# Kernel tuning notes

Measured on AMD Instinct MI355X. Metric: run time of the kernel, lower is better.

## Reference

```python
import jax, jax.numpy as jnp
import numpy as np

B, S, D, H = 2, 4096, 1024, 16
DK = D // H


def setup_inputs() -> dict:
    key = jax.random.key(0)
    ks = jax.random.split(key, 8)
    q = jax.random.normal(ks[0], (B, S, D), dtype=jnp.float32)
    k = jax.random.normal(ks[1], (B, S, D), dtype=jnp.float32)
    v = jax.random.normal(ks[2], (B, S, D), dtype=jnp.float32)
    mask = jax.random.randint(ks[3], (1, 1, S, S), 0, 2, dtype=jnp.int32)
    # torch.nn.Linear weights, y = x @ W.T ; Kaiming-uniform-ish init scale
    lim = 1.0 / np.sqrt(D)
    Wq = jax.random.uniform(ks[4], (D, D), jnp.float32, -lim, lim)
    Wk = jax.random.uniform(ks[5], (D, D), jnp.float32, -lim, lim)
    Wv = jax.random.uniform(ks[6], (D, D), jnp.float32, -lim, lim)
    Wo = jax.random.uniform(ks[7], (D, D), jnp.float32, -lim, lim)
    return {"q": q, "k": k, "v": v, "mask": mask,
            "Wq": Wq, "Wk": Wk, "Wv": Wv, "Wo": Wo}


def reference(q, k, v, mask, Wq, Wk, Wv, Wo):
    # Linear projections (torch Linear: x @ W.T), split into heads [B,H,S,DK]
    def heads(x, W):
        return (x @ W.T).reshape(B, S, H, DK).transpose(0, 2, 1, 3)

    Q, K, V = heads(q, Wq), heads(k, Wk), heads(v, Wv)
    scale = 1.0 / jnp.sqrt(jnp.asarray(DK, dtype=Q.dtype))
    # [B,H,S,S] score matrix (original materializes it fully)
    scores = jnp.einsum("bhqd,bhkd->bhqk", Q, K) * scale
    # NOTE: original calls masked_fill without assignment -> mask is a no-op.
    # Dropout: eval-mode identity (original also references missing self.dropout).
    attn = jax.nn.softmax(scores, axis=-1)
    out = jnp.einsum("bhqk,bhkd->bhqd", attn, V)  # [B,H,S,DK]
    out = out.transpose(0, 2, 1, 3).reshape(B, S, D)
    return out @ Wo.T
```

## Files before the change

### kernel.cpp

```cpp
#include <hip/hip_runtime.h>
#include <cstdint>
#include <cstddef>

using u16 = unsigned short;
using u32 = unsigned int;

typedef _Float16 f16x8 __attribute__((ext_vector_type(8)));
typedef float    f32x4 __attribute__((ext_vector_type(4)));
typedef float    f32x16 __attribute__((ext_vector_type(16)));

#define MFMA16(a,b,c) __builtin_amdgcn_mfma_f32_16x16x32_f16((a),(b),(c),0,0,0)
#define MFMA32(a,b,c) __builtin_amdgcn_mfma_f32_32x32x16_f16((a),(b),(c),0,0,0)

__device__ __forceinline__ u16 f2h(float f) {
  return __builtin_bit_cast(u16, (_Float16)f);
}
__device__ __forceinline__ u32 pkrtz(float a, float b) {
  return __builtin_bit_cast(u32, __builtin_amdgcn_cvt_pkrtz(a, b));
}
__device__ __forceinline__ void plswap(u32 &a, u32 &b) {
  asm volatile("v_permlane32_swap_b32 %0, %1" : "+v"(a), "+v"(b));
}
__device__ __forceinline__ void async16(const void* g, void* lds) {
  __builtin_amdgcn_global_load_lds((const __attribute__((address_space(1))) void*)g,
                                   (__attribute__((address_space(3))) void*)lds,
                                   16, 0, 0);
}
#if __has_builtin(__builtin_amdgcn_exp2f)
__device__ __forceinline__ float exp2_hw(float x) { return __builtin_amdgcn_exp2f(x); }
#else
__device__ __forceinline__ float exp2_hw(float x) {
  float r; asm("v_exp_f32 %0, %1" : "=v"(r) : "v"(x)); return r;
}
#endif

__global__ __launch_bounds__(256) void cvt_f32_f16(const float* __restrict__ in,
                                                   u16* __restrict__ out, int n4,
                                                   float scale) {
  int i = blockIdx.x * 256 + threadIdx.x;
  const int stride = gridDim.x * 256;
  for (; i < n4; i += stride) {
    const float4 f = reinterpret_cast<const float4*>(in)[i];
    ushort4 o;
    o.x = f2h(f.x * scale); o.y = f2h(f.y * scale);
    o.z = f2h(f.z * scale); o.w = f2h(f.w * scale);
    reinterpret_cast<ushort4*>(out)[i] = o;
  }
}

template <int OF32>
__global__ __launch_bounds__(256) void gemm_bt(const u16* __restrict__ A,
                                               const u16* __restrict__ Bw,
                                               float* __restrict__ Cf,
                                               u16* __restrict__ Ch,
                                               int M, int N, int K) {
  __shared__ __align__(16) u16 Asm[128 * 64];
  __shared__ __align__(16) u16 Bsm[128 * 64];
  const int tid = threadIdx.x;
  const int w = tid >> 6, l = tid & 63;
  const int wr = w >> 1, wc = w & 1;
  const int m0 = blockIdx.y * 128, n0 = blockIdx.x * 128;
  const int lr = l >> 3, lc = l & 7, csrc = lc ^ lr;
  const int laneq = l & 15, laneg = l >> 4;
  f32x4 acc[4][4] = {};
  for (int k0 = 0; k0 < K; k0 += 64) {
    __syncthreads();
#pragma unroll
    for (int c = 0; c < 4; ++c) {
      const int row = c * 32 + w * 8 + lr;
      async16(A + (size_t)(m0 + row) * K + k0 + csrc * 8, &Asm[c * 2048 + w * 512]);
      async16(Bw + (size_t)(n0 + row) * K + k0 + csrc * 8, &Bsm[c * 2048 + w * 512]);
    }
    __syncthreads();
#pragma unroll
    for (int ks = 0; ks < 2; ++ks) {
      f16x8 af[4], bfr[4];
#pragma unroll
      for (int mi = 0; mi < 4; ++mi) {
        const int row = wr * 64 + mi * 16 + laneq;
        const int ch = (ks * 4 + laneg) ^ (row & 7);
        af[mi] = *(const f16x8*)&Asm[row * 64 + ch * 8];
      }
#pragma unroll
      for (int ni = 0; ni < 4; ++ni) {
        const int row = wc * 64 + ni * 16 + laneq;
        const int ch = (ks * 4 + laneg) ^ (row & 7);
        bfr[ni] = *(const f16x8*)&Bsm[row * 64 + ch * 8];
      }
#pragma unroll
      for (int mi = 0; mi < 4; ++mi)
#pragma unroll
        for (int ni = 0; ni < 4; ++ni)
          acc[mi][ni] = MFMA16(af[mi], bfr[ni], acc[mi][ni]);
    }
  }
#pragma unroll
  for (int mi = 0; mi < 4; ++mi)
#pragma unroll
    for (int r = 0; r < 4; ++r) {
      const int gm = m0 + wr * 64 + mi * 16 + laneg * 4 + r;
#pragma unroll
      for (int ni = 0; ni < 4; ++ni) {
        const int gn = n0 + wc * 64 + ni * 16 + laneq;
        if constexpr (OF32) Cf[(size_t)gm * N + gn] = acc[mi][ni][r];
        else                Ch[(size_t)gm * N + gn] = f2h(acc[mi][ni][r]);
      }
    }
}

__global__ __launch_bounds__(256) void transpose_v(const u16* __restrict__ Vp,
                                                   u16* __restrict__ VT) {
  __shared__ u16 t[64 * 66];
  const int tid = threadIdx.x;
  const int s0 = blockIdx.x * 64, bh = blockIdx.y;
  const int b = bh >> 4, h = bh & 15;
  const int r = tid >> 2;
  const u16* src = Vp + (size_t)(b * 4096 + s0 + r) * 1024 + h * 64;
#pragma unroll
  for (int i = 0; i < 2; ++i) {
    const int c = (tid & 3) + i * 4;
    union { uint4 u; u32 ww[4]; } vv;
    vv.u = *(const uint4*)(src + c * 8);
#pragma unroll
    for (int j = 0; j < 4; ++j)
      *(u32*)&t[r * 66 + c * 8 + j * 2] = vv.ww[j];
  }
  __syncthreads();
  const int dk = tid >> 2;
  u16* dst = VT + ((size_t)bh * 64 + dk) * 4096 + s0;
#pragma unroll
  for (int i = 0; i < 2; ++i) {
    const int sc = (tid & 3) + i * 4;
    union { uint4 u; u16 s[8]; } o;
#pragma unroll
    for (int j = 0; j < 8; ++j) o.s[j] = t[(sc * 8 + j) * 66 + dk];
    *(uint4*)(dst + sc * 8) = o.u;
  }
}

__global__ __launch_bounds__(256, 4) void attn_fwd(const u16* __restrict__ Qp,
                                                   const u16* __restrict__ Kp,
                                                   const u16* __restrict__ VT,
                                                   u16* __restrict__ AO) {
  union SM {
    struct { u16 K[2][64 * 64]; u16 V[2][64 * 64]; } st;
    u16 osm[4][32 * 72];
  };
  __shared__ __align__(16) SM sm;
  const int tid = threadIdx.x, w = tid >> 6, l = tid & 63;
  const int l31 = l & 31, hi = l >> 5, l7 = l & 7, lr = l >> 3;
  const int bid = blockIdx.x;
  const int slot = bid >> 3;
  const int bh = (bid & 7) * 4 + (slot >> 5), qx = slot & 31;
  const int b = bh >> 4, h = bh & 15;
  const int q0 = qx * 128;
  const size_t hb = (size_t)b * 4096 * 1024 + (size_t)h * 64;
  const u16* Kh = Kp + hb;
  const u16* Vh = VT + (size_t)bh * 64 * 4096;
  const int csrc = l7 ^ lr;

  f16x8 qf[4];
  {
    const u16* qp = Qp + hb + (size_t)(q0 + w * 32 + l31) * 1024 + hi * 8;
#pragma unroll
    for (int kk = 0; kk < 4; ++kk) qf[kk] = *(const f16x8*)(qp + kk * 16);
  }

  f32x16 zero16;
#pragma unroll
  for (int r = 0; r < 16; ++r) zero16[r] = 0.f;
  f16x8 ones;
#pragma unroll
  for (int r = 0; r < 8; ++r) ones[r] = (_Float16)1.0f;

  f32x16 acc[2];
  f32x16 accl;
#pragma unroll
  for (int r = 0; r < 16; ++r) { acc[0][r] = 0.f; acc[1][r] = 0.f; accl[r] = 0.f; }

  int koff = (w * 8 + lr) * 1024 + csrc * 8;
  int voff = (w * 8 + lr) * 4096 + csrc * 8;

  async16(Kh + koff,             &sm.st.K[0][w * 512]);
  async16(Kh + koff + 32 * 1024, &sm.st.K[0][w * 512 + 2048]);
  async16(Vh + voff,             &sm.st.V[0][w * 512]);
  async16(Vh + voff + 32 * 4096, &sm.st.V[0][w * 512 + 2048]);

  for (int t = 0; t < 64; ++t) {
    const int cur = t & 1;
    __syncthreads();
    if (t < 63) {
      koff += 64 * 1024;
      voff += 64;
      async16(Kh + koff,             &sm.st.K[cur ^ 1][w * 512]);
      async16(Kh + koff + 32 * 1024, &sm.st.K[cur ^ 1][w * 512 + 2048]);
      async16(Vh + voff,             &sm.st.V[cur ^ 1][w * 512]);
      async16(Vh + voff + 32 * 4096, &sm.st.V[cur ^ 1][w * 512 + 2048]);
    }
    const u16* Ks = sm.st.K[cur];
    const u16* Vs = sm.st.V[cur];
#pragma unroll
    for (int kt = 0; kt < 2; ++kt) {
      __builtin_amdgcn_s_setprio(1);
      f16x8 kf = *(const f16x8*)&Ks[(kt * 32 + l31) * 64 + ((hi ^ l7) << 3)];
      f32x16 sv = MFMA32(kf, qf[0], zero16);
#pragma unroll
      for (int kk = 1; kk < 4; ++kk) {
        kf = *(const f16x8*)&Ks[(kt * 32 + l31) * 64 + (((kk * 2 + hi) ^ l7) << 3)];
        sv = MFMA32(kf, qf[kk], sv);
      }
      __builtin_amdgcn_s_setprio(0);
#pragma unroll
      for (int r = 0; r < 16; ++r) sv[r] = exp2_hw(sv[r]);
      f16x8 pf[2];
#pragma unroll
      for (int half = 0; half < 2; ++half) {
        const int rb = half * 8;
        u32 a0 = pkrtz(sv[rb + 0], sv[rb + 1]);
        u32 a1 = pkrtz(sv[rb + 2], sv[rb + 3]);
        u32 b0 = pkrtz(sv[rb + 4], sv[rb + 5]);
        u32 b1 = pkrtz(sv[rb + 6], sv[rb + 7]);
        plswap(a0, b0);
        plswap(a1, b1);
        union { u32 ww[4]; f16x8 v; } uu;
        uu.ww[0] = a0; uu.ww[1] = a1; uu.ww[2] = b0; uu.ww[3] = b1;
        pf[half] = uu.v;
      }
      __builtin_amdgcn_s_setprio(1);
#pragma unroll
      for (int half = 0; half < 2; ++half) {
        accl = MFMA32(ones, pf[half], accl);
#pragma unroll
        for (int ds = 0; ds < 2; ++ds) {
          const f16x8 vf = *(const f16x8*)&Vs[(ds * 32 + l31) * 64 + (((kt * 4 + half * 2 + hi) ^ l7) << 3)];
          acc[ds] = MFMA32(vf, pf[half], acc[ds]);
        }
      }
      __builtin_amdgcn_s_setprio(0);
    }
  }
  __syncthreads();
  {
    const float rn = 1.f / accl[0];
#pragma unroll
    for (int ds = 0; ds < 2; ++ds)
#pragma unroll
      for (int g = 0; g < 4; ++g) {
        uint2 val;
        val.x = pkrtz(acc[ds][4 * g + 0] * rn, acc[ds][4 * g + 1] * rn);
        val.y = pkrtz(acc[ds][4 * g + 2] * rn, acc[ds][4 * g + 3] * rn);
        *(uint2*)&sm.osm[w][l31 * 72 + ds * 32 + g * 8 + hi * 4] = val;
      }
  }
  asm volatile("s_waitcnt lgkmcnt(0)" ::: "memory");
#pragma unroll
  for (int i = 0; i < 4; ++i) {
    const int row = lr + i * 8;
    const uint4 vv = *(const uint4*)&sm.osm[w][row * 72 + l7 * 8];
    *(uint4*)(AO + hb + (size_t)(q0 + w * 32 + row) * 1024 + l7 * 8) = vv;
  }
}

extern "C" void kernel_launch(void* const* d_in, const int* in_sizes, int n_in,
                              void* d_out, int out_size, void* d_ws, size_t ws_size,
                              hipStream_t stream) {
  const float* q  = (const float*)d_in[0];
  const float* k  = (const float*)d_in[1];
  const float* v  = (const float*)d_in[2];
  const float* Wq = (const float*)d_in[4];
  const float* Wk = (const float*)d_in[5];
  const float* Wv = (const float*)d_in[6];
  const float* Wo = (const float*)d_in[7];
  float* out = (float*)d_out;

  char* ws = (char*)d_ws;
  u16* xb  = (u16*)ws;
  u16* wqb = (u16*)(ws + 16777216);
  u16* wkb = wqb + 1048576;
  u16* wvb = wkb + 1048576;
  u16* wob = wvb + 1048576;
  u16* Qp  = (u16*)(ws + 16777216 + 8388608);
  u16* Kpp = Qp + 8388608;
  u16* Vpp = Kpp + 8388608;
  u16* AO  = Vpp + 8388608;

  constexpr float SC = 0.125f * 1.44269504088896340736f;
  cvt_f32_f16<<<256, 256, 0, stream>>>(Wq, wqb, 262144, SC);
  cvt_f32_f16<<<256, 256, 0, stream>>>(Wk, wkb, 262144, 1.0f);
  cvt_f32_f16<<<256, 256, 0, stream>>>(Wv, wvb, 262144, 1.0f);
  cvt_f32_f16<<<256, 256, 0, stream>>>(Wo, wob, 262144, 1.0f);

  const dim3 gg(8, 64), gb(256);
  cvt_f32_f16<<<2048, 256, 0, stream>>>(q, xb, 2097152, 1.0f);
  gemm_bt<0><<<gg, gb, 0, stream>>>(xb, wqb, nullptr, Qp, 8192, 1024, 1024);
  cvt_f32_f16<<<2048, 256, 0, stream>>>(k, xb, 2097152, 1.0f);
  gemm_bt<0><<<gg, gb, 0, stream>>>(xb, wkb, nullptr, Kpp, 8192, 1024, 1024);
  cvt_f32_f16<<<2048, 256, 0, stream>>>(v, xb, 2097152, 1.0f);
  gemm_bt<0><<<gg, gb, 0, stream>>>(xb, wvb, nullptr, Vpp, 8192, 1024, 1024);

  transpose_v<<<dim3(64, 32), gb, 0, stream>>>(Vpp, xb);

  attn_fwd<<<1024, gb, 0, stream>>>(Qp, Kpp, xb, AO);

  gemm_bt<1><<<gg, gb, 0, stream>>>(AO, wob, out, nullptr, 8192, 1024, 1024);
}
```

Before: 307.9 us.

## Batch conversion and QK projection launches; compute V transposed directly via swapped GEMM

The four weight conversions and three input conversions are merged into two multi-tensor launches, and the Q and K projections run as one z-batched GEMM launch. The V projection is computed as Wv·xvᵀ (a 1024×8192 output), which yields V already transposed in [h*64+dk][b*4096+s] layout, so the separate transpose kernel goes away. Attention V indexing is updated to the new stride. This cuts launch count and the extra V read/write pass, at the cost of a larger workspace and a differently shaped V GEMM.

```diff
diff --git a/kernel.cpp b/kernel.cpp
--- a/kernel.cpp
+++ b/kernel.cpp
@@ -34,26 +34,52 @@
 }
 #endif
 
-__global__ __launch_bounds__(256) void cvt_f32_f16(const float* __restrict__ in,
-                                                   u16* __restrict__ out, int n4,
-                                                   float scale) {
+__global__ __launch_bounds__(256) void cvt4_w(const float* __restrict__ w0,
+                                              const float* __restrict__ w1,
+                                              const float* __restrict__ w2,
+                                              const float* __restrict__ w3,
+                                              u16* __restrict__ d0, u16* __restrict__ d1,
+                                              u16* __restrict__ d2, u16* __restrict__ d3,
+                                              int n4, float scale0) {
+  const int y = blockIdx.y;
+  const float* in = y == 0 ? w0 : (y == 1 ? w1 : (y == 2 ? w2 : w3));
+  u16* out = y == 0 ? d0 : (y == 1 ? d1 : (y == 2 ? d2 : d3));
+  const float sc = y == 0 ? scale0 : 1.0f;
   int i = blockIdx.x * 256 + threadIdx.x;
   const int stride = gridDim.x * 256;
   for (; i < n4; i += stride) {
     const float4 f = reinterpret_cast<const float4*>(in)[i];
     ushort4 o;
-    o.x = f2h(f.x * scale); o.y = f2h(f.y * scale);
-    o.z = f2h(f.z * scale); o.w = f2h(f.w * scale);
+    o.x = f2h(f.x * sc); o.y = f2h(f.y * sc);
+    o.z = f2h(f.z * sc); o.w = f2h(f.w * sc);
     reinterpret_cast<ushort4*>(out)[i] = o;
   }
 }
 
+__global__ __launch_bounds__(256) void cvt3_x(const float* __restrict__ q,
+                                              const float* __restrict__ k,
+                                              const float* __restrict__ v,
+                                              u16* __restrict__ xq, u16* __restrict__ xk,
+                                              u16* __restrict__ xv, int n4) {
+  const int y = blockIdx.y;
+  const float* in = y == 0 ? q : (y == 1 ? k : v);
+  u16* out = y == 0 ? xq : (y == 1 ? xk : xv);
+  int i = blockIdx.x * 256 + threadIdx.x;
+  const int stride = gridDim.x * 256;
+  for (; i < n4; i += stride) {
+    const float4 f = reinterpret_cast<const float4*>(in)[i];
+    ushort4 o;
+    o.x = f2h(f.x); o.y = f2h(f.y); o.z = f2h(f.z); o.w = f2h(f.w);
+    reinterpret_cast<ushort4*>(out)[i] = o;
+  }
+}
+
 template <int OF32>
-__global__ __launch_bounds__(256) void gemm_bt(const u16* __restrict__ A,
-                                               const u16* __restrict__ Bw,
-                                               float* __restrict__ Cf,
-                                               u16* __restrict__ Ch,
-                                               int M, int N, int K) {
+__device__ __forceinline__ void gemm_body(const u16* __restrict__ A,
+                                          const u16* __restrict__ Bw,
+                                          float* __restrict__ Cf,
+                                          u16* __restrict__ Ch,
+                                          int M, int N, int K) {
   __shared__ __align__(16) u16 Asm[128 * 64];
   __shared__ __align__(16) u16 Bsm[128 * 64];
   const int tid = threadIdx.x;
@@ -108,34 +134,28 @@
     }
 }
 
-__global__ __launch_bounds__(256) void transpose_v(const u16* __restrict__ Vp,
-                                                   u16* __restrict__ VT) {
-  __shared__ u16 t[64 * 66];
-  const int tid = threadIdx.x;
-  const int s0 = blockIdx.x * 64, bh = blockIdx.y;
-  const int b = bh >> 4, h = bh & 15;
-  const int r = tid >> 2;
-  const u16* src = Vp + (size_t)(b * 4096 + s0 + r) * 1024 + h * 64;
-#pragma unroll
-  for (int i = 0; i < 2; ++i) {
-    const int c = (tid & 3) + i * 4;
-    union { uint4 u; u32 ww[4]; } vv;
-    vv.u = *(const uint4*)(src + c * 8);
-#pragma unroll
-    for (int j = 0; j < 4; ++j)
-      *(u32*)&t[r * 66 + c * 8 + j * 2] = vv.ww[j];
-  }
-  __syncthreads();
-  const int dk = tid >> 2;
-  u16* dst = VT + ((size_t)bh * 64 + dk) * 4096 + s0;
-#pragma unroll
-  for (int i = 0; i < 2; ++i) {
-    const int sc = (tid & 3) + i * 4;
-    union { uint4 u; u16 s[8]; } o;
-#pragma unroll
-    for (int j = 0; j < 8; ++j) o.s[j] = t[(sc * 8 + j) * 66 + dk];
-    *(uint4*)(dst + sc * 8) = o.u;
-  }
+__global__ __launch_bounds__(256) void gemm_qk(const u16* __restrict__ xq,
+                                               const u16* __restrict__ wq,
+                                               u16* __restrict__ Qp,
+                                               const u16* __restrict__ xk,
+                                               const u16* __restrict__ wk,
+                                               u16* __restrict__ Kp) {
+  const bool zk = blockIdx.z != 0;
+  gemm_body<0>(zk ? xk : xq, zk ? wk : wq, nullptr, zk ? Kp : Qp, 8192, 1024, 1024);
+}
+
+__global__ __launch_bounds__(256) void gemm_h(const u16* __restrict__ A,
+                                              const u16* __restrict__ Bw,
+                                              u16* __restrict__ Ch,
+                                              int M, int N, int K) {
+  gemm_body<0>(A, Bw, nullptr, Ch, M, N, K);
+}
+
+__global__ __launch_bounds__(256) void gemm_f(const u16* __restrict__ A,
+                                              const u16* __restrict__ Bw,
+                                              float* __restrict__ Cf,
+                                              int M, int N, int K) {
+  gemm_body<1>(A, Bw, Cf, nullptr, M, N, K);
 }
 
 __global__ __launch_bounds__(256, 4) void attn_fwd(const u16* __restrict__ Qp,
@@ -156,7 +176,7 @@
   const int q0 = qx * 128;
   const size_t hb = (size_t)b * 4096 * 1024 + (size_t)h * 64;
   const u16* Kh = Kp + hb;
-  const u16* Vh = VT + (size_t)bh * 64 * 4096;
+  const u16* Vh = VT + (size_t)h * 64 * 8192 + (size_t)b * 4096;
   const int csrc = l7 ^ lr;
 
   f16x8 qf[4];
@@ -179,12 +199,12 @@
   for (int r = 0; r < 16; ++r) { acc[0][r] = 0.f; acc[1][r] = 0.f; accl[r] = 0.f; }
 
   int koff = (w * 8 + lr) * 1024 + csrc * 8;
-  int voff = (w * 8 + lr) * 4096 + csrc * 8;
+  int voff = (w * 8 + lr) * 8192 + csrc * 8;
 
   async16(Kh + koff,             &sm.st.K[0][w * 512]);
   async16(Kh + koff + 32 * 1024, &sm.st.K[0][w * 512 + 2048]);
   async16(Vh + voff,             &sm.st.V[0][w * 512]);
-  async16(Vh + voff + 32 * 4096, &sm.st.V[0][w * 512 + 2048]);
+  async16(Vh + voff + 32 * 8192, &sm.st.V[0][w * 512 + 2048]);
 
   for (int t = 0; t < 64; ++t) {
     const int cur = t & 1;
@@ -195,7 +215,7 @@
       async16(Kh + koff,             &sm.st.K[cur ^ 1][w * 512]);
       async16(Kh + koff + 32 * 1024, &sm.st.K[cur ^ 1][w * 512 + 2048]);
       async16(Vh + voff,             &sm.st.V[cur ^ 1][w * 512]);
-      async16(Vh + voff + 32 * 4096, &sm.st.V[cur ^ 1][w * 512 + 2048]);
+      async16(Vh + voff + 32 * 8192, &sm.st.V[cur ^ 1][w * 512 + 2048]);
     }
     const u16* Ks = sm.st.K[cur];
     const u16* Vs = sm.st.V[cur];
@@ -274,33 +294,27 @@
   float* out = (float*)d_out;
 
   char* ws = (char*)d_ws;
-  u16* xb  = (u16*)ws;
-  u16* wqb = (u16*)(ws + 16777216);
+  u16* xq  = (u16*)ws;
+  u16* xk  = (u16*)(ws + 16777216);
+  u16* xv  = (u16*)(ws + 2 * 16777216);
+  u16* Qp  = (u16*)(ws + 3 * 16777216);
+  u16* Kpp = (u16*)(ws + 4 * 16777216);
+  u16* wqb = (u16*)(ws + 5 * 16777216);
   u16* wkb = wqb + 1048576;
   u16* wvb = wkb + 1048576;
   u16* wob = wvb + 1048576;
-  u16* Qp  = (u16*)(ws + 16777216 + 8388608);
-  u16* Kpp = Qp + 8388608;
-  u16* Vpp = Kpp + 8388608;
-  u16* AO  = Vpp + 8388608;
+  u16* VT  = xq;
+  u16* AO  = xv;
 
   constexpr float SC = 0.125f * 1.44269504088896340736f;
-  cvt_f32_f16<<<256, 256, 0, stream>>>(Wq, wqb, 262144, SC);
-  cvt_f32_f16<<<256, 256, 0, stream>>>(Wk, wkb, 262144, 1.0f);
-  cvt_f32_f16<<<256, 256, 0, stream>>>(Wv, wvb, 262144, 1.0f);
-  cvt_f32_f16<<<256, 256, 0, stream>>>(Wo, wob, 262144, 1.0f);
-
-  const dim3 gg(8, 64), gb(256);
-  cvt_f32_f16<<<2048, 256, 0, stream>>>(q, xb, 2097152, 1.0f);
-  gemm_bt<0><<<gg, gb, 0, stream>>>(xb, wqb, nullptr, Qp, 8192, 1024, 1024);
-  cvt_f32_f16<<<2048, 256, 0, stream>>>(k, xb, 2097152, 1.0f);
-  gemm_bt<0><<<gg, gb, 0, stream>>>(xb, wkb, nullptr, Kpp, 8192, 1024, 1024);
-  cvt_f32_f16<<<2048, 256, 0, stream>>>(v, xb, 2097152, 1.0f);
-  gemm_bt<0><<<gg, gb, 0, stream>>>(xb, wvb, nullptr, Vpp, 8192, 1024, 1024);
-
-  transpose_v<<<dim3(64, 32), gb, 0, stream>>>(Vpp, xb);
-
-  attn_fwd<<<1024, gb, 0, stream>>>(Qp, Kpp, xb, AO);
-
-  gemm_bt<1><<<gg, gb, 0, stream>>>(AO, wob, out, nullptr, 8192, 1024, 1024);
-}
+  cvt4_w<<<dim3(256, 4), 256, 0, stream>>>(Wq, Wk, Wv, Wo, wqb, wkb, wvb, wob,
+                                           262144, SC);
+  cvt3_x<<<dim3(1024, 3), 256, 0, stream>>>(q, k, v, xq, xk, xv, 2097152);
+
+  gemm_qk<<<dim3(8, 64, 2), 256, 0, stream>>>(xq, wqb, Qp, xk, wkb, Kpp);
+  gemm_h<<<dim3(64, 8), 256, 0, stream>>>(wvb, xv, VT, 1024, 8192, 1024);
+
+  attn_fwd<<<1024, 256, 0, stream>>>(Qp, Kpp, VT, AO);
+
+  gemm_f<<<dim3(8, 64), 256, 0, stream>>>(AO, wob, out, 8192, 1024, 1024);
+}
```

After: 284.9 us. -7.5%, faster.
